# Optimization experiments

Measured on AMD Instinct MI355X. Metric: run time of the kernel, lower is better.

## Reference

```python
import jax, jax.numpy as jnp
import numpy as np

B, S, HID = 2, 2048, 2048
NH, NKV, D = 16, 8, 128
N_REP = NH // NKV
EPS = 1e-6
THETA = 10000.0


def setup_inputs() -> dict:
    key = jax.random.key(0)
    ks = jax.random.split(key, 6)
    s = 0.02
    return {
        "hidden_states": jax.random.normal(ks[0], (B, S, HID), jnp.float32),
        "attention_mask": jnp.ones((B, S), jnp.float32),
        "wq": jax.random.normal(ks[1], (HID, NH * D), jnp.float32) * s,
        "wk": jax.random.normal(ks[2], (HID, NKV * D), jnp.float32) * s,
        "wv": jax.random.normal(ks[3], (HID, NKV * D), jnp.float32) * s,
        "wo": jax.random.normal(ks[4], (NH * D, HID), jnp.float32) * s,
        "q_norm_w": jnp.ones((D,), jnp.float32),
        "k_norm_w": jnp.ones((D,), jnp.float32),
    }


def _rms_norm(x, w, eps=EPS):
    # x: (..., D); computed in fp32 like the torch module
    x32 = x.astype(jnp.float32)
    var = jnp.mean(x32 * x32, axis=-1, keepdims=True)
    return (w * (x32 * jax.lax.rsqrt(var + eps))).astype(x.dtype)


def _rotate_half(x):
    x1, x2 = jnp.split(x, 2, axis=-1)
    return jnp.concatenate((-x2, x1), axis=-1)


def _rope_cos_sin(seq_len, dim, dtype):
    inv_freq = 1.0 / (THETA ** (jnp.arange(0, dim, 2, dtype=jnp.float32) / dim))
    t = jnp.arange(seq_len, dtype=jnp.float32)
    freqs = t[:, None] * inv_freq[None, :]          # (S, D/2)
    emb = jnp.concatenate((freqs, freqs), axis=-1)  # (S, D)
    # broadcast to (1, 1, S, D)
    return jnp.cos(emb).astype(dtype)[None, None], jnp.sin(emb).astype(dtype)[None, None]


def reference(hidden_states, attention_mask, wq, wk, wv, wo, q_norm_w, k_norm_w):
    b, s, _ = hidden_states.shape
    # QKV projections (bias-free)
    q = (hidden_states @ wq).reshape(b, s, NH, D).transpose(0, 2, 1, 3)   # (b, nh, s, d)
    k = (hidden_states @ wk).reshape(b, s, NKV, D).transpose(0, 2, 1, 3)  # (b, nkv, s, d)
    v = (hidden_states @ wv).reshape(b, s, NKV, D).transpose(0, 2, 1, 3)
    # per-head QK RMSNorm
    q = _rms_norm(q, q_norm_w)
    k = _rms_norm(k, k_norm_w)
    # RoPE
    cos, sin = _rope_cos_sin(s, D, q.dtype)
    q = q * cos + _rotate_half(q) * sin
    k = k * cos + _rotate_half(k) * sin
    # GQA repeat kv heads
    k = jnp.repeat(k, N_REP, axis=1)
    v = jnp.repeat(v, N_REP, axis=1)
    # SDPA (bidirectional, additive padding mask)
    scale = 1.0 / np.sqrt(D)
    scores = jnp.einsum("bhqd,bhkd->bhqk", q, k) * scale
    add_mask = (1.0 - attention_mask)[:, None, None, :] * jnp.finfo(scores.dtype).min
    scores = scores + add_mask
    attn = jax.nn.softmax(scores, axis=-1)
    out = jnp.einsum("bhqk,bhkd->bhqd", attn, v)
    out = out.transpose(0, 2, 1, 3).reshape(b, s, NH * D)
    return out @ wo
```

## Files before the change

### kernel.cpp

```cpp
#include <hip/hip_runtime.h>
#include <stdint.h>

#define BB   2
#define SS   2048
#define HID  2048
#define NHQ  16
#define NKV  8
#define DD   128
#define QKVW 4096

typedef __bf16 v8bf   __attribute__((ext_vector_type(8)));
typedef float  f32x4  __attribute__((ext_vector_type(4)));
typedef float  f32x16 __attribute__((ext_vector_type(16)));

__device__ __forceinline__ float bf2f(ushort u) {
    union { unsigned int i; float f; } x; x.i = ((unsigned int)u) << 16; return x.f;
}
__device__ __forceinline__ ushort f2bf(float f) {
    union { float f; unsigned int i; } x; x.f = f;
    unsigned int i = x.i;
    return (ushort)((i + 0x7fffu + ((i >> 16) & 1u)) >> 16);
}
__device__ __forceinline__ v8bf as_bf8(uint4 u) { return __builtin_bit_cast(v8bf, u); }

__device__ __forceinline__ unsigned int cvtpk_bf16(float lo, float hi) {
    unsigned int r;
    asm("v_cvt_pk_bf16_f32 %0, %1, %2" : "=v"(r) : "v"(lo), "v"(hi));
    return r;
}

__device__ __forceinline__ void store_el(float* p, float v)  { *p = v; }
__device__ __forceinline__ void store_el(ushort* p, float v) { *p = f2bf(v); }

__device__ __forceinline__ void gll16(const ushort* g, ushort* l) {
    __builtin_amdgcn_global_load_lds(
        (const __attribute__((address_space(1))) void*)g,
        (__attribute__((address_space(3))) void*)l, 16, 0, 0);
}

__device__ __forceinline__ int swz_off(int r, int lcolb) {
    return r * 64 + (((lcolb) ^ ((r & 4) << 3)) >> 1);
}
__device__ __forceinline__ int hswz(int r, int colb) {
    return r * 32 + (((colb) ^ ((r & 8) << 2)) >> 1);
}

#define PREP_CAST   8192
#define PREP_WQ     (PREP_CAST)
#define PREP_WK     (PREP_WQ + 4096)
#define PREP_WV     (PREP_WK + 2048)
#define PREP_WO     (PREP_WV + 2048)
#define PREP_TOTAL  (PREP_WO + 4096)

__device__ __forceinline__ void tcast_body(
    const float* __restrict__ in, ushort* __restrict__ out,
    int K, int N, int bx, int by, int t)
{
    __shared__ float tile[32][33];
    int n0 = bx * 32, k0 = by * 32;
    int tx = t & 31, ty = t >> 5;
#pragma unroll
    for (int i = 0; i < 32; i += 8)
        tile[ty + i][tx] = in[(size_t)(k0 + ty + i) * N + n0 + tx];
    __syncthreads();
#pragma unroll
    for (int i = 0; i < 32; i += 8)
        out[(size_t)(n0 + ty + i) * K + k0 + tx] = f2bf(tile[tx][ty + i]);
}

__global__ __launch_bounds__(256) void prep(
    const float* __restrict__ X,  const float* __restrict__ wq,
    const float* __restrict__ wk, const float* __restrict__ wv,
    const float* __restrict__ wo,
    ushort* __restrict__ Xb, ushort* __restrict__ WqkvT, ushort* __restrict__ Wot)
{
    int bid = blockIdx.x, t = threadIdx.x;
    if (bid < PREP_CAST) {
        int i = (bid * 256 + t) * 4;
        float4 v = *(const float4*)&X[i];
        ushort4 o = { f2bf(v.x), f2bf(v.y), f2bf(v.z), f2bf(v.w) };
        *(ushort4*)&Xb[i] = o;
    } else if (bid < PREP_WK) {
        int l = bid - PREP_WQ;
        tcast_body(wq, WqkvT, 2048, 2048, l & 63, l >> 6, t);
    } else if (bid < PREP_WV) {
        int l = bid - PREP_WK;
        tcast_body(wk, WqkvT + (size_t)2048 * 2048, 2048, 1024, l & 31, l >> 5, t);
    } else if (bid < PREP_WO) {
        int l = bid - PREP_WV;
        tcast_body(wv, WqkvT + (size_t)3072 * 2048, 2048, 1024, l & 31, l >> 5, t);
    } else {
        int l = bid - PREP_WO;
        tcast_body(wo, Wot, 2048, 2048, l & 63, l >> 6, t);
    }
}

__global__ __launch_bounds__(512, 1) void gemm256(
    const ushort* __restrict__ A, const ushort* __restrict__ Bt,
    ushort* __restrict__ C, int M, int N, int K)
{
    __shared__ __align__(16) ushort As[2][2][256 * 32];
    __shared__ __align__(16) ushort Bs[2][2][256 * 32];
    const int t = threadIdx.x;
    const int lane = t & 63, wave = t >> 6;
    const int quad = lane >> 4, l15 = lane & 15;
    const int m0 = blockIdx.y * 256, n0 = blockIdx.x * 256;
    const int wm = (wave >> 1) * 64;
    const int wn = (wave & 1) * 128;

    const f32x4 zv = {0.f, 0.f, 0.f, 0.f};
    f32x4 acc[4][8];
#pragma unroll
    for (int i = 0; i < 4; i++)
#pragma unroll
        for (int j = 0; j < 8; j++) acc[i][j] = zv;

    int srow[2], scol[2];
#pragma unroll
    for (int j = 0; j < 2; j++) {
        int p16 = (j * 512 + t) * 16;
        int lg = p16 ^ (((p16 >> 9) & 1) << 5);
        srow[j] = lg >> 6; scol[j] = (lg & 63) >> 1;
    }
    int aoff[4], boff[8];
#pragma unroll
    for (int mf = 0; mf < 4; mf++) aoff[mf] = hswz(wm + mf * 16 + l15, quad * 16);
#pragma unroll
    for (int nf = 0; nf < 8; nf++) boff[nf] = hswz(wn + nf * 16 + l15, quad * 16);

#define STAGE_HALF(buf, hh, kb)                                                          \
    {                                                                                    \
        _Pragma("unroll")                                                                \
        for (int j = 0; j < 2; j++)                                                      \
            gll16(&A[(size_t)(m0 + srow[j]) * K + (kb) + scol[j]],                       \
                  &As[buf][hh][(j * 512 + t) * 8]);                                      \
        _Pragma("unroll")                                                                \
        for (int j = 0; j < 2; j++)                                                      \
            gll16(&Bt[(size_t)(n0 + srow[j]) * K + (kb) + scol[j]],                      \
                  &Bs[buf][hh][(j * 512 + t) * 8]);                                      \
    }

    const int NT = K >> 6;

    STAGE_HALF(0, 0, 0);
    STAGE_HALF(0, 1, 32);
    asm volatile("s_waitcnt vmcnt(4)" ::: "memory");
    __builtin_amdgcn_s_barrier();

    uint4 af[4], bf[4];
    for (int T = 0; T < NT; T++) {
        const int c = T & 1;
        const bool stg = (T + 1) < NT;
        const int kn = (T + 1) << 6;

#pragma unroll
        for (int mf = 0; mf < 4; mf++) af[mf] = *(const uint4*)&As[c][0][aoff[mf]];
#pragma unroll
        for (int nf = 0; nf < 4; nf++) bf[nf] = *(const uint4*)&Bs[c][0][boff[nf]];
        if (stg) STAGE_HALF(c ^ 1, 0, kn);
        __builtin_amdgcn_s_barrier();
        asm volatile("s_waitcnt lgkmcnt(0)" ::: "memory");
        __builtin_amdgcn_sched_barrier(0);
        __builtin_amdgcn_s_setprio(1);
#pragma unroll
        for (int mf = 0; mf < 4; mf++)
#pragma unroll
            for (int nf = 0; nf < 4; nf++)
                acc[mf][nf] = __builtin_amdgcn_mfma_f32_16x16x32_bf16(
                    as_bf8(af[mf]), as_bf8(bf[nf]), acc[mf][nf], 0, 0, 0);
        __builtin_amdgcn_s_setprio(0);
        __builtin_amdgcn_s_barrier();

#pragma unroll
        for (int nf = 0; nf < 4; nf++) bf[nf] = *(const uint4*)&Bs[c][0][boff[4 + nf]];
        __builtin_amdgcn_s_barrier();
        asm volatile("s_waitcnt lgkmcnt(0)" ::: "memory");
        __builtin_amdgcn_sched_barrier(0);
        __builtin_amdgcn_s_setprio(1);
#pragma unroll
        for (int mf = 0; mf < 4; mf++)
#pragma unroll
            for (int nf = 0; nf < 4; nf++)
                acc[mf][4 + nf] = __builtin_amdgcn_mfma_f32_16x16x32_bf16(
                    as_bf8(af[mf]), as_bf8(bf[nf]), acc[mf][4 + nf], 0, 0, 0);
        __builtin_amdgcn_s_setprio(0);
        if (stg) asm volatile("s_waitcnt vmcnt(4)" ::: "memory");
        else     asm volatile("s_waitcnt vmcnt(0)" ::: "memory");
        __builtin_amdgcn_s_barrier();

#pragma unroll
        for (int mf = 0; mf < 4; mf++) af[mf] = *(const uint4*)&As[c][1][aoff[mf]];
#pragma unroll
        for (int nf = 0; nf < 4; nf++) bf[nf] = *(const uint4*)&Bs[c][1][boff[nf]];
        if (stg) STAGE_HALF(c ^ 1, 1, kn + 32);
        __builtin_amdgcn_s_barrier();
        asm volatile("s_waitcnt lgkmcnt(0)" ::: "memory");
        __builtin_amdgcn_sched_barrier(0);
        __builtin_amdgcn_s_setprio(1);
#pragma unroll
        for (int mf = 0; mf < 4; mf++)
#pragma unroll
            for (int nf = 0; nf < 4; nf++)
                acc[mf][nf] = __builtin_amdgcn_mfma_f32_16x16x32_bf16(
                    as_bf8(af[mf]), as_bf8(bf[nf]), acc[mf][nf], 0, 0, 0);
        __builtin_amdgcn_s_setprio(0);
        __builtin_amdgcn_s_barrier();

#pragma unroll
        for (int nf = 0; nf < 4; nf++) bf[nf] = *(const uint4*)&Bs[c][1][boff[4 + nf]];
        __builtin_amdgcn_s_barrier();
        asm volatile("s_waitcnt lgkmcnt(0)" ::: "memory");
        __builtin_amdgcn_sched_barrier(0);
        __builtin_amdgcn_s_setprio(1);
#pragma unroll
        for (int mf = 0; mf < 4; mf++)
#pragma unroll
            for (int nf = 0; nf < 4; nf++)
                acc[mf][4 + nf] = __builtin_amdgcn_mfma_f32_16x16x32_bf16(
                    as_bf8(af[mf]), as_bf8(bf[nf]), acc[mf][4 + nf], 0, 0, 0);
        __builtin_amdgcn_s_setprio(0);
        if (stg) {
            asm volatile("s_waitcnt vmcnt(4)" ::: "memory");
            __builtin_amdgcn_s_barrier();
        }
    }
#undef STAGE_HALF

#pragma unroll
    for (int mf = 0; mf < 4; mf++)
#pragma unroll
        for (int nf = 0; nf < 8; nf++)
#pragma unroll
            for (int r = 0; r < 4; r++) {
                int row = m0 + wm + mf * 16 + quad * 4 + r;
                int col = n0 + wn + nf * 16 + l15;
                C[(size_t)row * N + col] = f2bf(acc[mf][nf][r]);
            }
}

template <typename OutT>
__global__ __launch_bounds__(512, 2) void gemm_bt2(
    const ushort* __restrict__ A, const ushort* __restrict__ Bt,
    OutT* __restrict__ C, int M, int N, int K)
{
    __shared__ __align__(16) ushort As[3][256 * 64];
    __shared__ __align__(16) ushort Bs[3][128 * 64];
    const int t = threadIdx.x;
    const int lane = t & 63, wave = t >> 6;
    const int quad = lane >> 4, l15 = lane & 15;
    const int m0 = blockIdx.y * 256, n0 = blockIdx.x * 128;
    const int wm = (wave >> 1) * 64;
    const int wn = (wave & 1) * 64;

    const f32x4 zv = {0.f, 0.f, 0.f, 0.f};
    f32x4 acc[4][4];
#pragma unroll
    for (int i = 0; i < 4; i++)
#pragma unroll
        for (int j = 0; j < 4; j++) acc[i][j] = zv;

    int arow[4], acol[4];
#pragma unroll
    for (int j = 0; j < 4; j++) {
        int p = (j * 512 + t) * 16;
        int l = p ^ (((p >> 9) & 1) << 5);
        arow[j] = l >> 7; acol[j] = (l & 127) >> 1;
    }
    int brow[2], bcol[2];
#pragma unroll
    for (int j = 0; j < 2; j++) {
        int p = (j * 512 + t) * 16;
        int l = p ^ (((p >> 9) & 1) << 5);
        brow[j] = l >> 7; bcol[j] = (l & 127) >> 1;
    }

    int aoff[4][2], boff[2][2][2];
#pragma unroll
    for (int mf = 0; mf < 4; mf++)
#pragma unroll
        for (int kk = 0; kk < 2; kk++)
            aoff[mf][kk] = swz_off(wm + mf * 16 + l15, kk * 64 + quad * 16);
#pragma unroll
    for (int q = 0; q < 2; q++)
#pragma unroll
        for (int nf = 0; nf < 2; nf++)
#pragma unroll
            for (int kk = 0; kk < 2; kk++)
                boff[q][nf][kk] = swz_off(wn + q * 32 + nf * 16 + l15, kk * 64 + quad * 16);

#define STAGE_A(j, slot, kk0) \
    gll16(&A[(size_t)(m0 + arow[j]) * K + (kk0) + acol[j]], &As[slot][0] + ((j) * 512 + t) * 8)
#define STAGE_B(j, slot, kk0) \
    gll16(&Bt[(size_t)(n0 + brow[j]) * K + (kk0) + bcol[j]], &Bs[slot][0] + ((j) * 512 + t) * 8)

    const int NT = K >> 6;

#pragma unroll
    for (int j = 0; j < 4; j++) STAGE_A(j, 0, 0);
#pragma unroll
    for (int j = 0; j < 2; j++) STAGE_B(j, 0, 0);
#pragma unroll
    for (int j = 0; j < 4; j++) STAGE_A(j, 1, 64);
#pragma unroll
    for (int j = 0; j < 2; j++) STAGE_B(j, 1, 64);
    asm volatile("s_waitcnt vmcnt(6)" ::: "memory");
    __builtin_amdgcn_s_barrier();

    int cur = 0;
    for (int T = 0; T < NT; T++) {
        const ushort* Ac = &As[cur][0];
        const ushort* Bc = &Bs[cur][0];
        int stg = cur + 2; if (stg >= 3) stg -= 3;
        const int k2 = (T + 2) << 6;
        const bool do_stage = (T + 2) < NT;

        uint4 af[4][2], bf[2][2];
#pragma unroll
        for (int mf = 0; mf < 4; mf++)
#pragma unroll
            for (int kk = 0; kk < 2; kk++)
                af[mf][kk] = *(const uint4*)&Ac[aoff[mf][kk]];
#pragma unroll
        for (int nf = 0; nf < 2; nf++)
#pragma unroll
            for (int kk = 0; kk < 2; kk++)
                bf[nf][kk] = *(const uint4*)&Bc[boff[0][nf][kk]];
        if (do_stage) {
            STAGE_A(0, stg, k2); STAGE_A(1, stg, k2); STAGE_B(0, stg, k2);
        }
        __builtin_amdgcn_s_barrier();
        asm volatile("s_waitcnt lgkmcnt(0)" ::: "memory");
        __builtin_amdgcn_sched_barrier(0);
        __builtin_amdgcn_s_setprio(1);
#pragma unroll
        for (int mf = 0; mf < 4; mf++)
#pragma unroll
            for (int nf = 0; nf < 2; nf++)
#pragma unroll
                for (int kk = 0; kk < 2; kk++)
                    acc[mf][nf] = __builtin_amdgcn_mfma_f32_16x16x32_bf16(
                        as_bf8(af[mf][kk]), as_bf8(bf[nf][kk]), acc[mf][nf], 0, 0, 0);
        __builtin_amdgcn_s_setprio(0);
        __builtin_amdgcn_s_barrier();

#pragma unroll
        for (int nf = 0; nf < 2; nf++)
#pragma unroll
            for (int kk = 0; kk < 2; kk++)
                bf[nf][kk] = *(const uint4*)&Bc[boff[1][nf][kk]];
        if (do_stage) {
            STAGE_A(2, stg, k2); STAGE_A(3, stg, k2); STAGE_B(1, stg, k2);
            asm volatile("s_waitcnt vmcnt(6)" ::: "memory");
        } else if (T + 2 == NT) {
            asm volatile("s_waitcnt vmcnt(0)" ::: "memory");
        }
        __builtin_amdgcn_s_barrier();
        asm volatile("s_waitcnt lgkmcnt(0)" ::: "memory");
        __builtin_amdgcn_sched_barrier(0);
        __builtin_amdgcn_s_setprio(1);
#pragma unroll
        for (int mf = 0; mf < 4; mf++)
#pragma unroll
            for (int nf = 0; nf < 2; nf++)
#pragma unroll
                for (int kk = 0; kk < 2; kk++)
                    acc[mf][2 + nf] = __builtin_amdgcn_mfma_f32_16x16x32_bf16(
                        as_bf8(af[mf][kk]), as_bf8(bf[nf][kk]), acc[mf][2 + nf], 0, 0, 0);
        __builtin_amdgcn_s_setprio(0);
        __builtin_amdgcn_s_barrier();

        cur++; if (cur == 3) cur = 0;
    }
#undef STAGE_A
#undef STAGE_B

#pragma unroll
    for (int mf = 0; mf < 4; mf++)
#pragma unroll
        for (int nf = 0; nf < 4; nf++)
#pragma unroll
            for (int r = 0; r < 4; r++) {
                int row = m0 + wm + mf * 16 + quad * 4 + r;
                int col = n0 + wn + nf * 16 + l15;
                store_el(&C[(size_t)row * N + col], acc[mf][nf][r]);
            }
}

__global__ __launch_bounds__(256) void norm_rope(
    ushort* __restrict__ qkv, const float* __restrict__ qw, const float* __restrict__ kw)
{
    int row = blockIdx.x;
    int s = row & (SS - 1);
    int lane = threadIdx.x & 63, wave = threadIdx.x >> 6;
    int l = lane & 31, hsel = lane >> 5;
    float d0 = (float)(2 * l), d1 = d0 + 1.0f;
    float inv0 = expf(-d0 * (1.0f / 64.0f) * 9.210340371976184f);
    float inv1 = expf(-d1 * (1.0f / 64.0f) * 9.210340371976184f);
    float c0, s0, c1, s1;
    sincosf((float)s * inv0, &s0, &c0);
    sincosf((float)s * inv1, &s1, &c1);
    float qw0 = qw[2 * l], qw1 = qw[2 * l + 1], qy0 = qw[2 * l + 64], qy1 = qw[2 * l + 65];
    float kw0 = kw[2 * l], kw1 = kw[2 * l + 1], ky0 = kw[2 * l + 64], ky1 = kw[2 * l + 65];

#pragma unroll
    for (int pass = 0; pass < 3; pass++) {
        int h = pass * 8 + wave * 2 + hsel;
        ushort* p = qkv + (size_t)row * QKVW + h * 128;
        unsigned int ulo = *(const unsigned int*)&p[2 * l];
        unsigned int uhi = *(const unsigned int*)&p[2 * l + 64];
        float x0 = bf2f((ushort)ulo), x1 = bf2f((ushort)(ulo >> 16));
        float y0 = bf2f((ushort)uhi), y1 = bf2f((ushort)(uhi >> 16));
        float ssum = x0 * x0 + x1 * x1 + y0 * y0 + y1 * y1;
#pragma unroll
        for (int xm = 1; xm < 32; xm <<= 1) ssum += __shfl_xor(ssum, xm, 64);
        float r = rsqrtf(ssum * (1.0f / 128.0f) + 1e-6f);
        bool isq = (h < 16);
        float w0 = isq ? qw0 : kw0, w1 = isq ? qw1 : kw1;
        float v0 = isq ? qy0 : ky0, v1 = isq ? qy1 : ky1;
        float sc = isq ? (0.08838834764831845f * 1.4426950408889634f) : 1.0f;
        float nx0 = w0 * (x0 * r), nx1 = w1 * (x1 * r);
        float ny0 = v0 * (y0 * r), ny1 = v1 * (y1 * r);
        float ox0 = (nx0 * c0 - ny0 * s0) * sc, ox1 = (nx1 * c1 - ny1 * s1) * sc;
        float oy0 = (ny0 * c0 + nx0 * s0) * sc, oy1 = (ny1 * c1 + nx1 * s1) * sc;
        *(unsigned int*)&p[2 * l]      = (unsigned int)f2bf(ox0) | ((unsigned int)f2bf(ox1) << 16);
        *(unsigned int*)&p[2 * l + 64] = (unsigned int)f2bf(oy0) | ((unsigned int)f2bf(oy1) << 16);
    }
}

__global__ __launch_bounds__(256, 2) void flash_attn(
    const ushort* __restrict__ qkv, const float* __restrict__ mask, ushort* __restrict__ O)
{
    __shared__ __align__(16) ushort Ks[2][64 * 128];
    __shared__ __align__(16) ushort Vt[128 * 64];
    __shared__ __align__(16) float  Madd[SS];
    const int t = threadIdx.x;
    const int lane = t & 63, wave = t >> 6;
    const int l31 = lane & 31, half = lane >> 5;
    const int b = blockIdx.z, h = blockIdx.y, q0 = blockIdx.x * 128;
    const int kh = h >> 1;

#pragma unroll
    for (int i = 0; i < 2; i++) {
        int idx = i * 1024 + t * 4;
        float4 mv = *(const float4*)&mask[b * SS + idx];
        float4 o = { (1.f - mv.x) * -1e30f, (1.f - mv.y) * -1e30f,
                     (1.f - mv.z) * -1e30f, (1.f - mv.w) * -1e30f };
        *(float4*)&Madd[idx] = o;
    }

    uint4 aq[8];
    {
        const ushort* qp = qkv + ((size_t)(b * SS + q0 + wave * 32 + l31)) * QKVW + h * 128 + half * 8;
#pragma unroll
        for (int kt = 0; kt < 8; kt++) aq[kt] = *(const uint4*)&qp[kt * 16];
    }
    f32x16 acc_o[4];
#pragma unroll
    for (int i = 0; i < 4; i++)
#pragma unroll
        for (int r = 0; r < 16; r++) acc_o[i][r] = 0.f;
    float lp[4] = {0.f, 0.f, 0.f, 0.f};

    const ushort* Kg = qkv + (size_t)b * SS * QKVW + 2048 + kh * 128;
    const ushort* Vg = qkv + (size_t)b * SS * QKVW + 3072 + kh * 128;

    const int vp = t & 31, vdc = t >> 5;
    uint4 vreg[4];
#define LOAD_V(K0)                                                                  \
    {                                                                               \
        _Pragma("unroll")                                                           \
        for (int pass = 0; pass < 2; pass++) {                                      \
            int d0 = (vdc + pass * 8) * 8;                                          \
            vreg[pass * 2 + 0] = *(const uint4*)&Vg[(size_t)((K0) + 2 * vp) * QKVW + d0];     \
            vreg[pass * 2 + 1] = *(const uint4*)&Vg[(size_t)((K0) + 2 * vp + 1) * QKVW + d0]; \
        }                                                                           \
    }
#define STAGE_K(K0, buf)                                                            \
    {                                                                               \
        _Pragma("unroll")                                                           \
        for (int i = 0; i < 4; i++) {                                               \
            int chunk = i * 256 + t;                                                \
            int row = chunk >> 4, cp = chunk & 15;                                  \
            int cl = cp ^ (row & 15);                                               \
            gll16(&Kg[(size_t)((K0) + row) * QKVW + cl * 8], &Ks[buf][chunk * 8]);  \
        }                                                                           \
    }

    STAGE_K(0, 0);
    LOAD_V(0);

    for (int k0 = 0; k0 < SS; k0 += 64) {
        const int cur = (k0 >> 6) & 1;
        __syncthreads();
        if (k0 + 64 < SS) STAGE_K(k0 + 64, cur ^ 1);
#pragma unroll
        for (int pass = 0; pass < 2; pass++) {
            const ushort* pa_ = (const ushort*)&vreg[pass * 2 + 0];
            const ushort* pb_ = (const ushort*)&vreg[pass * 2 + 1];
            int d0 = (vdc + pass * 8) * 8;
#pragma unroll
            for (int j = 0; j < 8; j++) {
                int cp = (vp >> 2) ^ j;
                unsigned int v = (unsigned int)pa_[j] | ((unsigned int)pb_[j] << 16);
                *(unsigned int*)&Vt[(d0 + j) * 64 + cp * 8 + (vp & 3) * 2] = v;
            }
        }
        if (k0 + 64 < SS) LOAD_V(k0 + 64);
        asm volatile("s_waitcnt lgkmcnt(0)" ::: "memory");
        __builtin_amdgcn_sched_barrier(0);
        __builtin_amdgcn_s_barrier();

        f32x16 sc[2];
#pragma unroll
        for (int nt = 0; nt < 2; nt++)
#pragma unroll
            for (int g = 0; g < 4; g++) {
                f32x4 em = *(const f32x4*)&Madd[k0 + nt * 32 + 4 * half + g * 8];
#pragma unroll
                for (int j = 0; j < 4; j++) sc[nt][g * 4 + j] = em[j];
            }
        __builtin_amdgcn_s_setprio(1);
#pragma unroll
        for (int nt = 0; nt < 2; nt++) {
#pragma unroll
            for (int kt = 0; kt < 8; kt++) {
                int cp = (kt * 2 + half) ^ (l31 & 15);
                uint4 bk = *(const uint4*)&Ks[cur][(nt * 32 + l31) * 128 + cp * 8];
                sc[nt] = __builtin_amdgcn_mfma_f32_32x32x16_bf16(
                    as_bf8(bk), as_bf8(aq[kt]), sc[nt], 0, 0, 0);
            }
        }
        __builtin_amdgcn_s_setprio(0);

        uint4 pa[4];
#pragma unroll
        for (int nt = 0; nt < 2; nt++) {
            float p[16];
#pragma unroll
            for (int r = 0; r < 16; r++) {
                float pv = __builtin_amdgcn_exp2f(sc[nt][r]);
                p[r] = pv;
                lp[r & 3] += pv;
            }
            unsigned int pk[8];
#pragma unroll
            for (int i = 0; i < 8; i++) pk[i] = cvtpk_bf16(p[2 * i], p[2 * i + 1]);
            auto sA = __builtin_amdgcn_permlane32_swap(pk[0], pk[2], false, false);
            auto sB = __builtin_amdgcn_permlane32_swap(pk[1], pk[3], false, false);
            auto sC = __builtin_amdgcn_permlane32_swap(pk[4], pk[6], false, false);
            auto sD = __builtin_amdgcn_permlane32_swap(pk[5], pk[7], false, false);
            uint4 f0, f1;
            f0.x = sA[0]; f0.y = sB[0]; f0.z = sA[1]; f0.w = sB[1];
            f1.x = sC[0]; f1.y = sD[0]; f1.z = sC[1]; f1.w = sD[1];
            pa[nt * 2 + 0] = f0;
            pa[nt * 2 + 1] = f1;
        }

        __builtin_amdgcn_s_setprio(1);
#pragma unroll
        for (int kt2 = 0; kt2 < 4; kt2++) {
            int kc = kt2 * 2 + half;
            int co = (kc ^ (l31 & 7)) * 8;
#pragma unroll
            for (int nt = 0; nt < 4; nt++) {
                uint4 bv = *(const uint4*)&Vt[(nt * 32 + l31) * 64 + co];
                acc_o[nt] = __builtin_amdgcn_mfma_f32_32x32x16_bf16(
                    as_bf8(pa[kt2]), as_bf8(bv), acc_o[nt], 0, 0, 0);
            }
        }
        __builtin_amdgcn_s_setprio(0);
    }
    float lsum = (lp[0] + lp[1]) + (lp[2] + lp[3]);
    lsum += __shfl_xor(lsum, 32, 64);
    float linv = 1.0f / lsum;
    float li[16];
#pragma unroll
    for (int r = 0; r < 16; r++)
        li[r] = __shfl(linv, (r & 3) + 8 * (r >> 2) + 4 * half, 64);
#pragma unroll
    for (int nt = 0; nt < 4; nt++)
#pragma unroll
        for (int r = 0; r < 16; r++) {
            int prow = (r & 3) + 8 * (r >> 2) + 4 * half;
            int qrow = q0 + wave * 32 + prow;
            int d = nt * 32 + l31;
            float v = acc_o[nt][r] * li[r];
            O[((size_t)(b * SS + qrow)) * (NHQ * DD) + h * 128 + d] = f2bf(v);
        }
}

extern "C" void kernel_launch(void* const* d_in, const int* in_sizes, int n_in,
                              void* d_out, int out_size, void* d_ws, size_t ws_size,
                              hipStream_t stream)
{
    const float* X    = (const float*)d_in[0];
    const float* mask = (const float*)d_in[1];
    const float* wq   = (const float*)d_in[2];
    const float* wk   = (const float*)d_in[3];
    const float* wv   = (const float*)d_in[4];
    const float* wo   = (const float*)d_in[5];
    const float* qnw  = (const float*)d_in[6];
    const float* knw  = (const float*)d_in[7];
    float* out = (float*)d_out;

    const size_t M = (size_t)BB * SS;
    ushort* Xb    = (ushort*)d_ws;
    ushort* WqkvT = Xb    + M * HID;
    ushort* Wot   = WqkvT + (size_t)4096 * HID;
    ushort* QKV   = Wot   + (size_t)2048 * 2048;
    ushort* Obuf  = QKV   + M * QKVW;

    prep<<<PREP_TOTAL, 256, 0, stream>>>(X, wq, wk, wv, wo, Xb, WqkvT, Wot);

    gemm256<<<dim3(4096 / 256, 4096 / 256), 512, 0, stream>>>(Xb, WqkvT, QKV, 4096, 4096, 2048);

    norm_rope<<<(int)M, 256, 0, stream>>>(QKV, qnw, knw);

    flash_attn<<<dim3(SS / 128, NHQ, BB), 256, 0, stream>>>(QKV, mask, Obuf);

    gemm_bt2<float><<<dim3(2048 / 128, 4096 / 256), 512, 0, stream>>>(Obuf, Wot, out, 4096, 2048, 2048);
}
```

Measured before the change: 340.6 us.

## Split attention waves across key halves and reuse K/V fragments across two query tiles

Each wave now handles 64 query rows (two 32-row subtiles) against one 32-key half of each 64-key block, instead of 32 query rows against all 64 keys. Every K and V fragment read from LDS feeds two MFMAs, which halves LDS read traffic per MFMA. The two key-half waves then combine their partial outputs and row sums through LDS (reusing the K buffer) before the final normalisation and store. In exchange, accumulator registers double, which may hurt occupancy under launch_bounds(256,2), and the epilogue adds extra barriers and LDS exchange traffic.

```diff
diff --git a/kernel.cpp b/kernel.cpp
--- a/kernel.cpp
+++ b/kernel.cpp
@@ -436,6 +436,8 @@
     const int t = threadIdx.x;
     const int lane = t & 63, wave = t >> 6;
     const int l31 = lane & 31, half = lane >> 5;
+    const int qg = wave >> 1;
+    const int kh2 = wave & 1;
     const int b = blockIdx.z, h = blockIdx.y, q0 = blockIdx.x * 128;
     const int kh = h >> 1;
 
@@ -448,18 +450,26 @@
         *(float4*)&Madd[idx] = o;
     }
 
-    uint4 aq[8];
-    {
-        const ushort* qp = qkv + ((size_t)(b * SS + q0 + wave * 32 + l31)) * QKVW + h * 128 + half * 8;
-#pragma unroll
-        for (int kt = 0; kt < 8; kt++) aq[kt] = *(const uint4*)&qp[kt * 16];
-    }
-    f32x16 acc_o[4];
-#pragma unroll
-    for (int i = 0; i < 4; i++)
-#pragma unroll
-        for (int r = 0; r < 16; r++) acc_o[i][r] = 0.f;
-    float lp[4] = {0.f, 0.f, 0.f, 0.f};
+    uint4 aq[2][8];
+#pragma unroll
+    for (int s = 0; s < 2; s++) {
+        const ushort* qp = qkv + ((size_t)(b * SS + q0 + qg * 64 + s * 32 + l31)) * QKVW
+                         + h * 128 + half * 8;
+#pragma unroll
+        for (int kt = 0; kt < 8; kt++) aq[s][kt] = *(const uint4*)&qp[kt * 16];
+    }
+    f32x16 acc_o[2][4];
+#pragma unroll
+    for (int s = 0; s < 2; s++)
+#pragma unroll
+        for (int i = 0; i < 4; i++)
+#pragma unroll
+            for (int r = 0; r < 16; r++) acc_o[s][i][r] = 0.f;
+    float lp[2][4];
+#pragma unroll
+    for (int s = 0; s < 2; s++)
+#pragma unroll
+        for (int j = 0; j < 4; j++) lp[s][j] = 0.f;
 
     const ushort* Kg = qkv + (size_t)b * SS * QKVW + 2048 + kh * 128;
     const ushort* Vg = qkv + (size_t)b * SS * QKVW + 3072 + kh * 128;
@@ -512,35 +522,35 @@
 
         f32x16 sc[2];
 #pragma unroll
-        for (int nt = 0; nt < 2; nt++)
-#pragma unroll
-            for (int g = 0; g < 4; g++) {
-                f32x4 em = *(const f32x4*)&Madd[k0 + nt * 32 + 4 * half + g * 8];
-#pragma unroll
-                for (int j = 0; j < 4; j++) sc[nt][g * 4 + j] = em[j];
+        for (int g = 0; g < 4; g++) {
+            f32x4 em = *(const f32x4*)&Madd[k0 + kh2 * 32 + 4 * half + g * 8];
+#pragma unroll
+            for (int j = 0; j < 4; j++) {
+                sc[0][g * 4 + j] = em[j];
+                sc[1][g * 4 + j] = em[j];
             }
-        __builtin_amdgcn_s_setprio(1);
-#pragma unroll
-        for (int nt = 0; nt < 2; nt++) {
-#pragma unroll
-            for (int kt = 0; kt < 8; kt++) {
-                int cp = (kt * 2 + half) ^ (l31 & 15);
-                uint4 bk = *(const uint4*)&Ks[cur][(nt * 32 + l31) * 128 + cp * 8];
-                sc[nt] = __builtin_amdgcn_mfma_f32_32x32x16_bf16(
-                    as_bf8(bk), as_bf8(aq[kt]), sc[nt], 0, 0, 0);
-            }
-        }
-        __builtin_amdgcn_s_setprio(0);
-
-        uint4 pa[4];
-#pragma unroll
-        for (int nt = 0; nt < 2; nt++) {
+        }
+        __builtin_amdgcn_s_setprio(1);
+#pragma unroll
+        for (int kt = 0; kt < 8; kt++) {
+            int cp = (kt * 2 + half) ^ (l31 & 15);
+            uint4 bk = *(const uint4*)&Ks[cur][(kh2 * 32 + l31) * 128 + cp * 8];
+            sc[0] = __builtin_amdgcn_mfma_f32_32x32x16_bf16(
+                as_bf8(bk), as_bf8(aq[0][kt]), sc[0], 0, 0, 0);
+            sc[1] = __builtin_amdgcn_mfma_f32_32x32x16_bf16(
+                as_bf8(bk), as_bf8(aq[1][kt]), sc[1], 0, 0, 0);
+        }
+        __builtin_amdgcn_s_setprio(0);
+
+        uint4 pa[2][2];
+#pragma unroll
+        for (int s = 0; s < 2; s++) {
             float p[16];
 #pragma unroll
             for (int r = 0; r < 16; r++) {
-                float pv = __builtin_amdgcn_exp2f(sc[nt][r]);
+                float pv = __builtin_amdgcn_exp2f(sc[s][r]);
                 p[r] = pv;
-                lp[r & 3] += pv;
+                lp[s][r & 3] += pv;
             }
             unsigned int pk[8];
 #pragma unroll
@@ -552,41 +562,82 @@
             uint4 f0, f1;
             f0.x = sA[0]; f0.y = sB[0]; f0.z = sA[1]; f0.w = sB[1];
             f1.x = sC[0]; f1.y = sD[0]; f1.z = sC[1]; f1.w = sD[1];
-            pa[nt * 2 + 0] = f0;
-            pa[nt * 2 + 1] = f1;
-        }
-
-        __builtin_amdgcn_s_setprio(1);
-#pragma unroll
-        for (int kt2 = 0; kt2 < 4; kt2++) {
-            int kc = kt2 * 2 + half;
+            pa[s][0] = f0;
+            pa[s][1] = f1;
+        }
+
+        __builtin_amdgcn_s_setprio(1);
+#pragma unroll
+        for (int kt2 = 0; kt2 < 2; kt2++) {
+            int kc = kh2 * 4 + kt2 * 2 + half;
             int co = (kc ^ (l31 & 7)) * 8;
 #pragma unroll
             for (int nt = 0; nt < 4; nt++) {
                 uint4 bv = *(const uint4*)&Vt[(nt * 32 + l31) * 64 + co];
-                acc_o[nt] = __builtin_amdgcn_mfma_f32_32x32x16_bf16(
-                    as_bf8(pa[kt2]), as_bf8(bv), acc_o[nt], 0, 0, 0);
+                acc_o[0][nt] = __builtin_amdgcn_mfma_f32_32x32x16_bf16(
+                    as_bf8(pa[0][kt2]), as_bf8(bv), acc_o[0][nt], 0, 0, 0);
+                acc_o[1][nt] = __builtin_amdgcn_mfma_f32_32x32x16_bf16(
+                    as_bf8(pa[1][kt2]), as_bf8(bv), acc_o[1][nt], 0, 0, 0);
             }
         }
         __builtin_amdgcn_s_setprio(0);
     }
-    float lsum = (lp[0] + lp[1]) + (lp[2] + lp[3]);
-    lsum += __shfl_xor(lsum, 32, 64);
-    float linv = 1.0f / lsum;
-    float li[16];
-#pragma unroll
-    for (int r = 0; r < 16; r++)
-        li[r] = __shfl(linv, (r & 3) + 8 * (r >> 2) + 4 * half, 64);
-#pragma unroll
-    for (int nt = 0; nt < 4; nt++)
-#pragma unroll
-        for (int r = 0; r < 16; r++) {
-            int prow = (r & 3) + 8 * (r >> 2) + 4 * half;
-            int qrow = q0 + wave * 32 + prow;
-            int d = nt * 32 + l31;
-            float v = acc_o[nt][r] * li[r];
-            O[((size_t)(b * SS + qrow)) * (NHQ * DD) + h * 128 + d] = f2bf(v);
-        }
+
+    float lsum[2];
+#pragma unroll
+    for (int s = 0; s < 2; s++) {
+        float x = (lp[s][0] + lp[s][1]) + (lp[s][2] + lp[s][3]);
+        x += __shfl_xor(x, 32, 64);
+        lsum[s] = x;
+    }
+
+    float* Xch = (float*)&Ks[0][0];
+#pragma unroll
+    for (int s = 0; s < 2; s++) {
+        __syncthreads();
+        if (kh2) {
+#pragma unroll
+            for (int nt = 0; nt < 4; nt++)
+#pragma unroll
+                for (int r = 0; r < 16; r++)
+                    Xch[qg * 4096 + nt * 1024 + r * 64 + lane] = acc_o[s][nt][r];
+        }
+        __syncthreads();
+        if (!kh2) {
+#pragma unroll
+            for (int nt = 0; nt < 4; nt++)
+#pragma unroll
+                for (int r = 0; r < 16; r++)
+                    acc_o[s][nt][r] += Xch[qg * 4096 + nt * 1024 + r * 64 + lane];
+        }
+    }
+    __syncthreads();
+    if (kh2) {
+        Xch[(qg * 2 + 0) * 64 + lane] = lsum[0];
+        Xch[(qg * 2 + 1) * 64 + lane] = lsum[1];
+    }
+    __syncthreads();
+    if (!kh2) {
+#pragma unroll
+        for (int s = 0; s < 2; s++) {
+            float ltot = lsum[s] + Xch[(qg * 2 + s) * 64 + lane];
+            float linv = 1.0f / ltot;
+            float li[16];
+#pragma unroll
+            for (int r = 0; r < 16; r++)
+                li[r] = __shfl(linv, (r & 3) + 8 * (r >> 2) + 4 * half, 64);
+#pragma unroll
+            for (int nt = 0; nt < 4; nt++)
+#pragma unroll
+                for (int r = 0; r < 16; r++) {
+                    int prow = (r & 3) + 8 * (r >> 2) + 4 * half;
+                    int qrow = q0 + qg * 64 + s * 32 + prow;
+                    int d = nt * 32 + l31;
+                    float v = acc_o[s][nt][r] * li[r];
+                    O[((size_t)(b * SS + qrow)) * (NHQ * DD) + h * 128 + d] = f2bf(v);
+                }
+        }
+    }
 }
 
 extern "C" void kernel_launch(void* const* d_in, const int* in_sizes, int n_in,
```

Result: slower. 431.8 us (+26.8%).

## Fuse QK RMSNorm and RoPE into QKV GEMM epilogue with precomputed table

Applied to the files above, without the earlier changes.

Drops the standalone norm_rope kernel and applies per-head RMSNorm, RoPE and the softmax scale inside the epilogue of the QKV GEMM, while the accumulators are still in registers. Each wave's 128-column span is exactly one head, so the sum of squares is reduced with 16-lane shuffles. A cos/sin table is precomputed in the prep kernel and read from global memory in the epilogue. This removes a kernel launch and a full read-modify-write pass over the Q/K activations, at the cost of extra epilogue registers and table loads in a kernel already built for one block per CU.

```diff
diff --git a/kernel.cpp b/kernel.cpp
--- a/kernel.cpp
+++ b/kernel.cpp
@@ -50,7 +50,8 @@
 #define PREP_WK     (PREP_WQ + 4096)
 #define PREP_WV     (PREP_WK + 2048)
 #define PREP_WO     (PREP_WV + 2048)
-#define PREP_TOTAL  (PREP_WO + 4096)
+#define PREP_ROPE   (PREP_WO + 4096)
+#define PREP_TOTAL  (PREP_ROPE + 512)
 
 __device__ __forceinline__ void tcast_body(
     const float* __restrict__ in, ushort* __restrict__ out,
@@ -72,7 +73,8 @@
     const float* __restrict__ X,  const float* __restrict__ wq,
     const float* __restrict__ wk, const float* __restrict__ wv,
     const float* __restrict__ wo,
-    ushort* __restrict__ Xb, ushort* __restrict__ WqkvT, ushort* __restrict__ Wot)
+    ushort* __restrict__ Xb, ushort* __restrict__ WqkvT, ushort* __restrict__ Wot,
+    float2* __restrict__ rtab)
 {
     int bid = blockIdx.x, t = threadIdx.x;
     if (bid < PREP_CAST) {
@@ -89,15 +91,24 @@
     } else if (bid < PREP_WO) {
         int l = bid - PREP_WV;
         tcast_body(wv, WqkvT + (size_t)3072 * 2048, 2048, 1024, l & 31, l >> 5, t);
-    } else {
+    } else if (bid < PREP_ROPE) {
         int l = bid - PREP_WO;
         tcast_body(wo, Wot, 2048, 2048, l & 63, l >> 6, t);
+    } else {
+        int e = (bid - PREP_ROPE) * 256 + t;
+        int s = e >> 6, dp = e & 63;
+        float inv = expf(-(float)dp * (1.0f / 64.0f) * 9.210340371976184f);
+        float sn, cs;
+        sincosf((float)s * inv, &sn, &cs);
+        rtab[e] = make_float2(cs, sn);
     }
 }
 
 __global__ __launch_bounds__(512, 1) void gemm256(
     const ushort* __restrict__ A, const ushort* __restrict__ Bt,
-    ushort* __restrict__ C, int M, int N, int K)
+    ushort* __restrict__ C, int M, int N, int K,
+    const float* __restrict__ qnw, const float* __restrict__ knw,
+    const float2* __restrict__ rtab)
 {
     __shared__ __align__(16) ushort As[2][2][256 * 32];
     __shared__ __align__(16) ushort Bs[2][2][256 * 32];
@@ -226,16 +237,51 @@
     }
 #undef STAGE_HALF
 
-#pragma unroll
-    for (int mf = 0; mf < 4; mf++)
-#pragma unroll
-        for (int nf = 0; nf < 8; nf++)
+    const int col0 = n0 + wn;
+    if (col0 >= 3072) {
+#pragma unroll
+        for (int mf = 0; mf < 4; mf++)
+#pragma unroll
+            for (int nf = 0; nf < 8; nf++)
+#pragma unroll
+                for (int r = 0; r < 4; r++) {
+                    int row = m0 + wm + mf * 16 + quad * 4 + r;
+                    C[(size_t)row * N + col0 + nf * 16 + l15] = f2bf(acc[mf][nf][r]);
+                }
+    } else {
+        const bool isq = col0 < 2048;
+        const float* nw = isq ? qnw : knw;
+        const float scl = isq ? (0.08838834764831845f * 1.4426950408889634f) : 1.0f;
+        float wgt[8];
+#pragma unroll
+        for (int nf = 0; nf < 8; nf++) wgt[nf] = nw[nf * 16 + l15];
+#pragma unroll
+        for (int mf = 0; mf < 4; mf++)
 #pragma unroll
             for (int r = 0; r < 4; r++) {
                 int row = m0 + wm + mf * 16 + quad * 4 + r;
-                int col = n0 + wn + nf * 16 + l15;
-                C[(size_t)row * N + col] = f2bf(acc[mf][nf][r]);
+                float v[8];
+#pragma unroll
+                for (int nf = 0; nf < 8; nf++) v[nf] = acc[mf][nf][r];
+                float sum = 0.f;
+#pragma unroll
+                for (int nf = 0; nf < 8; nf++) sum = fmaf(v[nf], v[nf], sum);
+#pragma unroll
+                for (int xm = 1; xm < 16; xm <<= 1) sum += __shfl_xor(sum, xm, 64);
+                float rr = rsqrtf(sum * (1.0f / 128.0f) + 1e-6f);
+                int s = row & (SS - 1);
+#pragma unroll
+                for (int nf0 = 0; nf0 < 4; nf0++) {
+                    float2 cs = rtab[s * 64 + nf0 * 16 + l15];
+                    float x = v[nf0] * rr * wgt[nf0];
+                    float y = v[nf0 + 4] * rr * wgt[nf0 + 4];
+                    C[(size_t)row * N + col0 + nf0 * 16 + l15] =
+                        f2bf((x * cs.x - y * cs.y) * scl);
+                    C[(size_t)row * N + col0 + 64 + nf0 * 16 + l15] =
+                        f2bf((y * cs.x + x * cs.y) * scl);
+                }
             }
+    }
 }
 
 template <typename OutT>
@@ -386,47 +432,6 @@
             }
 }
 
-__global__ __launch_bounds__(256) void norm_rope(
-    ushort* __restrict__ qkv, const float* __restrict__ qw, const float* __restrict__ kw)
-{
-    int row = blockIdx.x;
-    int s = row & (SS - 1);
-    int lane = threadIdx.x & 63, wave = threadIdx.x >> 6;
-    int l = lane & 31, hsel = lane >> 5;
-    float d0 = (float)(2 * l), d1 = d0 + 1.0f;
-    float inv0 = expf(-d0 * (1.0f / 64.0f) * 9.210340371976184f);
-    float inv1 = expf(-d1 * (1.0f / 64.0f) * 9.210340371976184f);
-    float c0, s0, c1, s1;
-    sincosf((float)s * inv0, &s0, &c0);
-    sincosf((float)s * inv1, &s1, &c1);
-    float qw0 = qw[2 * l], qw1 = qw[2 * l + 1], qy0 = qw[2 * l + 64], qy1 = qw[2 * l + 65];
-    float kw0 = kw[2 * l], kw1 = kw[2 * l + 1], ky0 = kw[2 * l + 64], ky1 = kw[2 * l + 65];
-
-#pragma unroll
-    for (int pass = 0; pass < 3; pass++) {
-        int h = pass * 8 + wave * 2 + hsel;
-        ushort* p = qkv + (size_t)row * QKVW + h * 128;
-        unsigned int ulo = *(const unsigned int*)&p[2 * l];
-        unsigned int uhi = *(const unsigned int*)&p[2 * l + 64];
-        float x0 = bf2f((ushort)ulo), x1 = bf2f((ushort)(ulo >> 16));
-        float y0 = bf2f((ushort)uhi), y1 = bf2f((ushort)(uhi >> 16));
-        float ssum = x0 * x0 + x1 * x1 + y0 * y0 + y1 * y1;
-#pragma unroll
-        for (int xm = 1; xm < 32; xm <<= 1) ssum += __shfl_xor(ssum, xm, 64);
-        float r = rsqrtf(ssum * (1.0f / 128.0f) + 1e-6f);
-        bool isq = (h < 16);
-        float w0 = isq ? qw0 : kw0, w1 = isq ? qw1 : kw1;
-        float v0 = isq ? qy0 : ky0, v1 = isq ? qy1 : ky1;
-        float sc = isq ? (0.08838834764831845f * 1.4426950408889634f) : 1.0f;
-        float nx0 = w0 * (x0 * r), nx1 = w1 * (x1 * r);
-        float ny0 = v0 * (y0 * r), ny1 = v1 * (y1 * r);
-        float ox0 = (nx0 * c0 - ny0 * s0) * sc, ox1 = (nx1 * c1 - ny1 * s1) * sc;
-        float oy0 = (ny0 * c0 + nx0 * s0) * sc, oy1 = (ny1 * c1 + nx1 * s1) * sc;
-        *(unsigned int*)&p[2 * l]      = (unsigned int)f2bf(ox0) | ((unsigned int)f2bf(ox1) << 16);
-        *(unsigned int*)&p[2 * l + 64] = (unsigned int)f2bf(oy0) | ((unsigned int)f2bf(oy1) << 16);
-    }
-}
-
 __global__ __launch_bounds__(256, 2) void flash_attn(
     const ushort* __restrict__ qkv, const float* __restrict__ mask, ushort* __restrict__ O)
 {
@@ -609,12 +614,12 @@
     ushort* Wot   = WqkvT + (size_t)4096 * HID;
     ushort* QKV   = Wot   + (size_t)2048 * 2048;
     ushort* Obuf  = QKV   + M * QKVW;
-
-    prep<<<PREP_TOTAL, 256, 0, stream>>>(X, wq, wk, wv, wo, Xb, WqkvT, Wot);
-
-    gemm256<<<dim3(4096 / 256, 4096 / 256), 512, 0, stream>>>(Xb, WqkvT, QKV, 4096, 4096, 2048);
-
-    norm_rope<<<(int)M, 256, 0, stream>>>(QKV, qnw, knw);
+    float2* rtab  = (float2*)(Obuf + M * (size_t)(NHQ * DD));
+
+    prep<<<PREP_TOTAL, 256, 0, stream>>>(X, wq, wk, wv, wo, Xb, WqkvT, Wot, rtab);
+
+    gemm256<<<dim3(4096 / 256, 4096 / 256), 512, 0, stream>>>(
+        Xb, WqkvT, QKV, 4096, 4096, 2048, qnw, knw, rtab);
 
     flash_attn<<<dim3(SS / 128, NHQ, BB), 256, 0, stream>>>(QKV, mask, Obuf);
 
```

After: 333.1 us. -2.2%, faster.
